# Optimization experiments

Hardware: AMD Instinct MI355X
Metric: run time of the kernel (lower is better)

Reference implementation:

```python
import jax, jax.numpy as jnp
import numpy as np

B, T, C = 4, 1024, 1024
H, LAT = 16, 512
E, K, F = 8, 2, 1024
N_SHARED = 2
EPS = 1e-6
HD = C // H


def setup_inputs() -> dict:
    key = jax.random.key(0)
    ks = jax.random.split(key, 20)
    s = 0.02
    inp = {
        'x': jax.random.normal(ks[0], (B, T, C), jnp.float32),
        'g_attn': jnp.ones((C,), jnp.float32),
        'wq': jax.random.normal(ks[1], (C, H * HD), jnp.float32) * s,
        'wkv_down': jax.random.normal(ks[2], (C, LAT), jnp.float32) * s,
        'wk_up': jax.random.normal(ks[3], (LAT, HD), jnp.float32) * s,
        'wv_up': jax.random.normal(ks[4], (LAT, HD), jnp.float32) * s,
        'wo': jax.random.normal(ks[5], (H * HD, C), jnp.float32) * s,
        'g_moe': jnp.ones((C,), jnp.float32),
        'wr': jax.random.normal(ks[6], (C, E), jnp.float32) * s,
        'rb': jnp.zeros((E,), jnp.float32),
        'e_w1': jax.random.normal(ks[7], (E, C, F), jnp.float32) * s,
        'e_w2': jax.random.normal(ks[8], (E, F, C), jnp.float32) * s,
        'e_w3': jax.random.normal(ks[9], (E, C, F), jnp.float32) * s,
        's_w1': jax.random.normal(ks[10], (C, F * N_SHARED), jnp.float32) * s,
        's_w2': jax.random.normal(ks[11], (F * N_SHARED, C), jnp.float32) * s,
        's_w3': jax.random.normal(ks[12], (C, F * N_SHARED), jnp.float32) * s,
    }
    return inp


def _rmsnorm(x, g):
    ms = jnp.mean(jnp.square(x), axis=-1, keepdims=True)
    return x * jax.lax.rsqrt(ms + EPS) * g


def reference(x, g_attn, wq, wkv_down, wk_up, wv_up, wo, g_moe, wr, rb,
              e_w1, e_w2, e_w3, s_w1, s_w2, s_w3):
    # ---- MLA attention (no rope / no kv-cache path: freqs_cis=None, start_pos=None) ----
    xn = _rmsnorm(x, g_attn)
    q = (xn @ wq).reshape(B, T, H, HD)          # [B,T,H,hd]
    kv = xn @ wkv_down                            # [B,T,LAT]
    k = kv @ wk_up                                # [B,T,hd] shared across heads
    v = kv @ wv_up                                # [B,T,hd]
    scores = jnp.einsum('bthd,bsd->bhts', q, k) / jnp.sqrt(jnp.float32(HD))
    causal = jnp.tril(jnp.ones((T, T), dtype=bool))
    scores = jnp.where(causal, scores, -jnp.inf)
    p = jax.nn.softmax(scores, axis=-1)
    y = jnp.einsum('bhts,bsd->bthd', p, v).reshape(B, T, C) @ wo
    h = x + y

    # ---- DeepSeekMoE: top-k routing + masked softmax + experts + shared experts ----
    hn = _rmsnorm(h, g_moe)
    N = B * T
    xf = hn.reshape(N, C)
    logits = (xf @ wr) * (1.0 / jnp.sqrt(jnp.float32(C)))   # original logits
    biased = logits + rb
    _, idx = jax.lax.top_k(biased, K)                        # [N,K]
    mask = jnp.zeros((N, E), dtype=bool).at[jnp.arange(N)[:, None], idx].set(True)
    # softmax over only the selected logits; unselected -> 0 weight
    wfull = jax.nn.softmax(jnp.where(mask, logits, -jnp.inf), axis=-1)  # [N,E]

    # experts: SwiGLU FFN per expert (original computes each expert on all tokens)
    hid = jnp.einsum('nd,edf->enf', xf, e_w1) * jax.nn.silu(jnp.einsum('nd,edf->enf', xf, e_w3))
    moe_out = jnp.einsum('enf,efd,ne->nd', hid, e_w2, wfull)  # weighted combine

    shared = ((xf @ s_w1) * jax.nn.silu(xf @ s_w3)) @ s_w2
    out = h + (moe_out + shared).reshape(B, T, C)
    return out
```

## Files before the change

kernel.cpp:

```cpp
#include <hip/hip_runtime.h>
#include <hip/hip_bf16.h>

using bf16 = __hip_bfloat16;
typedef __attribute__((ext_vector_type(8))) short short8;
typedef __attribute__((ext_vector_type(4))) float f32x4;

static __device__ __forceinline__ float bf2f(bf16 v) { return __bfloat162float(v); }
static __device__ __forceinline__ bf16 f2bf(float v) { return __float2bfloat16(v); }

constexpr int CB = 4, CT = 1024, CC = 1024, CH = 16, CHD = 64, CLAT = 512;
constexpr int CE = 8, CF = 1024, CNS = 2;
constexpr int NTOK = CB * CT;
constexpr int FUP = CE * CF + CNS * CF;

struct alignas(8) bf16x4 { bf16 a, b, c, d; };

__global__ void pack_t_kernel(const float* __restrict__ src, bf16* __restrict__ dst,
                              int K, int N, int lddst, long srcZ, long dstZ, long plane) {
  __shared__ float tile[32][33];
  src += (long)blockIdx.z * srcZ;
  dst += (long)blockIdx.z * dstZ;
  int k0 = blockIdx.y * 32, n0 = blockIdx.x * 32;
  int tx = threadIdx.x, ty = threadIdx.y;
#pragma unroll
  for (int i = 0; i < 32; i += 8) {
    int k = k0 + ty + i, n = n0 + tx;
    tile[ty + i][tx] = (k < K && n < N) ? src[(long)k * N + n] : 0.f;
  }
  __syncthreads();
#pragma unroll
  for (int i = 0; i < 32; i += 8) {
    int n = n0 + ty + i, k = k0 + tx;
    if (n < N && k < K) {
      float v = tile[tx][ty + i];
      bf16 hi = f2bf(v);
      long idx = (long)n * lddst + k;
      dst[idx] = hi;
      if (plane) dst[idx + plane] = f2bf(v - bf2f(hi));
    }
  }
}

template<bool SPLIT>
__global__ void rmsnorm_kernel(const float* __restrict__ x, const float* __restrict__ g,
                               bf16* __restrict__ ob, long plane) {
  int row = blockIdx.x;
  int t = threadIdx.x;
  const float4* xr = (const float4*)(x + (long)row * CC);
  float4 v = xr[t];
  float ss = v.x * v.x + v.y * v.y + v.z * v.z + v.w * v.w;
#pragma unroll
  for (int o = 32; o > 0; o >>= 1) ss += __shfl_down(ss, o);
  __shared__ float wsum[4];
  if ((t & 63) == 0) wsum[t >> 6] = ss;
  __syncthreads();
  float tot = wsum[0] + wsum[1] + wsum[2] + wsum[3];
  float r = rsqrtf(tot * (1.f / CC) + 1e-6f);
  const float4* gr = (const float4*)g;
  float4 gv = gr[t];
  float o0 = v.x * r * gv.x, o1 = v.y * r * gv.y, o2 = v.z * r * gv.z, o3 = v.w * r * gv.w;
  long base = (long)row * CC + t * 4;
  bf16x4 hv = {f2bf(o0), f2bf(o1), f2bf(o2), f2bf(o3)};
  *(bf16x4*)(ob + base) = hv;
  if (SPLIT) {
    bf16x4 lv = {f2bf(o0 - bf2f(hv.a)), f2bf(o1 - bf2f(hv.b)),
                 f2bf(o2 - bf2f(hv.c)), f2bf(o3 - bf2f(hv.d))};
    *(bf16x4*)(ob + plane + base) = lv;
  }
}

__global__ void router_kernel(const float* __restrict__ hb, const float* __restrict__ g,
                              const float* __restrict__ wr, const float* __restrict__ rb,
                              float* __restrict__ wf) {
  int n = blockIdx.x, l = threadIdx.x;
  const float* hrow = hb + (long)n * CC;
  float xs[16];
  float ss = 0.f;
#pragma unroll
  for (int i = 0; i < 16; i++) {
    float xv = hrow[i * 64 + l];
    xs[i] = xv;
    ss += xv * xv;
  }
#pragma unroll
  for (int o = 32; o > 0; o >>= 1) ss += __shfl_xor(ss, o);
  float r = rsqrtf(ss * (1.f / CC) + 1e-6f);
  float acc[CE];
#pragma unroll
  for (int e = 0; e < CE; e++) acc[e] = 0.f;
#pragma unroll
  for (int i = 0; i < 16; i++) {
    int c = i * 64 + l;
    float v = xs[i] * r * g[c];
    const float* w = wr + (long)c * CE;
#pragma unroll
    for (int e = 0; e < CE; e++) acc[e] += v * w[e];
  }
#pragma unroll
  for (int e = 0; e < CE; e++)
#pragma unroll
    for (int o = 32; o > 0; o >>= 1) acc[e] += __shfl_down(acc[e], o);
  if (l == 0) {
    float lg[CE], bi[CE];
#pragma unroll
    for (int e = 0; e < CE; e++) { lg[e] = acc[e] * (1.f / 32.f); bi[e] = lg[e] + rb[e]; }
    int i1 = 0;
#pragma unroll
    for (int e = 1; e < CE; e++) if (bi[e] > bi[i1]) i1 = e;
    int i2 = -1;
#pragma unroll
    for (int e = 0; e < CE; e++) if (e != i1 && (i2 < 0 || bi[e] > bi[i2])) i2 = e;
    float mx = fmaxf(lg[i1], lg[i2]);
    float e1 = expf(lg[i1] - mx), e2 = expf(lg[i2] - mx);
    float inv = 1.f / (e1 + e2);
#pragma unroll
    for (int e = 0; e < CE; e++) wf[(long)n * CE + e] = 0.f;
    wf[(long)n * CE + i1] = e1 * inv;
    wf[(long)n * CE + i2] = e2 * inv;
  }
}

__global__ void softmax_kernel(bf16* __restrict__ scp, long plane) {
  int wid = threadIdx.x >> 6, l = threadIdx.x & 63;
  long rowid = (long)blockIdx.x * 4 + wid;
  int t = (int)(rowid & (CT - 1));
  bf16* row = scp + rowid * CT;
  int len = t + 1;
  float v[16];
  float m = -1e30f;
#pragma unroll
  for (int ii = 0; ii < 16; ii++) {
    int i = ii * 64 + l;
    v[ii] = (i < len) ? (bf2f(row[i]) + bf2f(row[i + plane])) * 0.125f : -1e30f;
    m = fmaxf(m, v[ii]);
  }
#pragma unroll
  for (int o = 32; o > 0; o >>= 1) m = fmaxf(m, __shfl_xor(m, o));
  float s = 0.f;
#pragma unroll
  for (int ii = 0; ii < 16; ii++) { v[ii] = expf(v[ii] - m); s += v[ii]; }
#pragma unroll
  for (int o = 32; o > 0; o >>= 1) s += __shfl_xor(s, o);
  float inv = 1.f / s;
#pragma unroll
  for (int ii = 0; ii < 16; ii++) {
    int i = ii * 64 + l;
    float pv = v[ii] * inv;
    bf16 hi = f2bf(pv);
    row[i] = hi;
    row[i + plane] = f2bf(pv - bf2f(hi));
  }
}

constexpr int EPI_SPLIT = 1, EPI_ADD = 2, EPI_KV = 3, EPI_SWIGLU = 4;

template<int BN, int EPI, int MODE>
__global__ __launch_bounds__(256) void gemm_bt(
    const bf16* __restrict__ A, long lda, long planeA,
    const bf16* __restrict__ B1, const bf16* __restrict__ B3, long ldb,
    void* __restrict__ Cv, long ldc, long planeC,
    int M, int N, int K,
    int zdiv, long sAz1, long sAz2, long sBz1, long sBz2, long sCz1, long sCz2,
    const float* __restrict__ aux1, void* __restrict__ aux2, int causal) {
  constexpr int BM = 128, BK = 32;
  constexpr int PA = (MODE == 1) ? 2 : 1;
  constexpr int PB = (MODE == 0) ? 1 : 2;
  constexpr int WN = (BN == 128) ? 2 : 1;
  constexpr int WM = 4 / WN;
  constexpr int FM = BM / (16 * WM);
  constexpr int FN = BN / (16 * WN);
  constexpr int ITA = (BM * BK / 8) / 256;
  constexpr int ITB = (BN * BK / 8) / 256;
  constexpr int A3 = (MODE == 2) ? FM : 1;
  constexpr int B3N = (MODE == 2) ? FN : 1;

  __shared__ bf16 As[PA][BM][BK];
  __shared__ bf16 Bs[PB][BN][BK];

  int z = blockIdx.z;
  int z1 = z / zdiv, z2 = z % zdiv;
  long offA = (long)z1 * sAz1 + (long)z2 * sAz2;
  long offB = (long)z1 * sBz1 + (long)z2 * sBz2;
  long offC = (long)z1 * sCz1 + (long)z2 * sCz2;

  int m0 = blockIdx.y * BM;
  int n0 = blockIdx.x * BN;
  if (causal && n0 > m0 + (BM - 1)) return;

  int tid = threadIdx.x;
  int wid = tid >> 6, lane = tid & 63;
  int wrow = (wid / WN) * (BM / WM);
  int wcol = (wid % WN) * (BN / WN);
  int lr = lane & 15, lk8 = (lane >> 4) * 8;

  const bf16* Ap0 = A + offA;
  const bf16* Ap1 = Ap0 + planeA;
  const bf16* Bp0 = B1 + offB;
  const bf16* Bp1 = B3 + offB;

  f32x4 acc[FM][FN] = {};
  f32x4 acc3[A3][B3N] = {};

  for (int k0 = 0; k0 < K; k0 += BK) {
    __syncthreads();
#pragma unroll
    for (int p = 0; p < PA; p++) {
      const bf16* Ap = p ? Ap1 : Ap0;
#pragma unroll
      for (int i = 0; i < ITA; i++) {
        int c = i * 256 + wid * 64 + lane;
        int r = c >> 2;
        int kc = (c & 3) * 8;
        __builtin_amdgcn_global_load_lds(
            (const __attribute__((address_space(1))) void*)(const void*)(Ap + (long)(m0 + r) * lda + (k0 + kc)),
            (__attribute__((address_space(3))) void*)(void*)(&As[p][0][0] + (i * 256 + wid * 64) * 8),
            16, 0, 0);
      }
    }
#pragma unroll
    for (int p = 0; p < PB; p++) {
      const bf16* Bp = p ? Bp1 : Bp0;
#pragma unroll
      for (int i = 0; i < ITB; i++) {
        int c = i * 256 + wid * 64 + lane;
        int r = c >> 2;
        int kc = (c & 3) * 8;
        __builtin_amdgcn_global_load_lds(
            (const __attribute__((address_space(1))) void*)(const void*)(Bp + (long)(n0 + r) * ldb + (k0 + kc)),
            (__attribute__((address_space(3))) void*)(void*)(&Bs[p][0][0] + (i * 256 + wid * 64) * 8),
            16, 0, 0);
      }
    }
    __syncthreads();

    short8 av[PA][FM], bv[PB][FN];
#pragma unroll
    for (int p = 0; p < PA; p++)
#pragma unroll
      for (int m = 0; m < FM; m++)
        av[p][m] = *(const short8*)&As[p][wrow + m * 16 + lr][lk8];
#pragma unroll
    for (int p = 0; p < PB; p++)
#pragma unroll
      for (int n = 0; n < FN; n++)
        bv[p][n] = *(const short8*)&Bs[p][wcol + n * 16 + lr][lk8];

#pragma unroll
    for (int m = 0; m < FM; m++)
#pragma unroll
      for (int n = 0; n < FN; n++) {
        if constexpr (MODE == 0) {
          acc[m][n] = __builtin_amdgcn_mfma_f32_16x16x32_bf16(av[0][m], bv[0][n], acc[m][n], 0, 0, 0);
        } else if constexpr (MODE == 1) {
          acc[m][n] = __builtin_amdgcn_mfma_f32_16x16x32_bf16(av[0][m], bv[0][n], acc[m][n], 0, 0, 0);
          acc[m][n] = __builtin_amdgcn_mfma_f32_16x16x32_bf16(av[0][m], bv[1][n], acc[m][n], 0, 0, 0);
          acc[m][n] = __builtin_amdgcn_mfma_f32_16x16x32_bf16(av[1][m], bv[0][n], acc[m][n], 0, 0, 0);
        } else {
          acc[m][n]  = __builtin_amdgcn_mfma_f32_16x16x32_bf16(av[0][m], bv[0][n], acc[m][n], 0, 0, 0);
          acc3[m][n] = __builtin_amdgcn_mfma_f32_16x16x32_bf16(av[0][m], bv[1][n], acc3[m][n], 0, 0, 0);
        }
      }
  }

#pragma unroll
  for (int m = 0; m < FM; m++)
#pragma unroll
    for (int n = 0; n < FN; n++) {
      int col = n0 + wcol + n * 16 + lr;
      if (col < N) {
#pragma unroll
        for (int r = 0; r < 4; r++) {
          int row = m0 + wrow + m * 16 + (lane >> 4) * 4 + r;
          float val = acc[m][n][r];
          if constexpr (EPI == EPI_SPLIT) {
            bf16 hi = f2bf(val);
            long ci = offC + (long)row * ldc + col;
            ((bf16*)Cv)[ci] = hi;
            ((bf16*)Cv)[ci + planeC] = f2bf(val - bf2f(hi));
          } else if constexpr (EPI == EPI_ADD) {
            long ci = (long)row * ldc + col;
            ((float*)Cv)[ci] = aux1[ci] + val;
          } else if constexpr (EPI == EPI_KV) {
            bf16 hi = f2bf(val);
            bf16 lo = f2bf(val - bf2f(hi));
            if (col < CHD) {
              long ci = (long)row * CHD + col;
              ((bf16*)Cv)[ci] = hi;
              ((bf16*)Cv)[ci + 262144] = lo;
            } else {
              int d = col - CHD;
              long vi = ((long)(row >> 10) * CHD + d) * CT + (row & (CT - 1));
              ((bf16*)aux2)[vi] = hi;
              ((bf16*)aux2)[vi + 262144] = lo;
            }
          } else if constexpr (EPI == EPI_SWIGLU) {
            float g3 = (MODE == 2) ? acc3[m][n][r] : 0.f;
            float sl = g3 / (1.f + expf(-g3));
            float wt = (col < CE * CF) ? aux1[(long)row * CE + (col >> 10)] : 1.f;
            ((bf16*)Cv)[(long)row * ldc + col] = f2bf(val * sl * wt);
          }
        }
      }
    }
}

extern "C" void kernel_launch(void* const* d_in, const int* in_sizes, int n_in,
                              void* d_out, int out_size, void* d_ws, size_t ws_size,
                              hipStream_t stream) {
  (void)in_sizes; (void)n_in; (void)out_size; (void)ws_size;
  const float* x        = (const float*)d_in[0];
  const float* g_attn   = (const float*)d_in[1];
  const float* wq       = (const float*)d_in[2];
  const float* wkv_down = (const float*)d_in[3];
  const float* wk_up    = (const float*)d_in[4];
  const float* wv_up    = (const float*)d_in[5];
  const float* wo       = (const float*)d_in[6];
  const float* g_moe    = (const float*)d_in[7];
  const float* wr       = (const float*)d_in[8];
  const float* rb       = (const float*)d_in[9];
  const float* e_w1     = (const float*)d_in[10];
  const float* e_w2     = (const float*)d_in[11];
  const float* e_w3     = (const float*)d_in[12];
  const float* s_w1     = (const float*)d_in[13];
  const float* s_w2     = (const float*)d_in[14];
  const float* s_w3     = (const float*)d_in[15];
  float* out = (float*)d_out;

  char* base = (char*)d_ws;
  bf16*  WqT    = (bf16*)(base + 0);
  bf16*  WkvT   = (bf16*)(base + 4194304);
  bf16*  WkvupT = (bf16*)(base + 6291456);
  bf16*  WoT    = (bf16*)(base + 6553600);
  bf16*  W1T    = (bf16*)(base + 10747904);
  bf16*  W3T    = (bf16*)(base + 31719424);
  bf16*  W2T    = (bf16*)(base + 52690944);
  float* hb     = (float*)(base + 73662464);
  float* wful   = (float*)(base + 90439680);
  char*  AR     = base + 90570752;
  bf16* xn  = (bf16*)(AR + 0);
  bf16* qb  = (bf16*)(AR + 16777216);
  bf16* kb  = (bf16*)(AR + 33554432);
  bf16* vt  = (bf16*)(AR + 34603008);
  bf16* scp = (bf16*)(AR + 35651584);
  bf16* kvb = scp;
  bf16* yb  = xn;
  bf16* hnb = (bf16*)(AR + 0);
  bf16* hid = (bf16*)(AR + 8388608);

  dim3 pblk(32, 8);
  auto packl = [&](const float* src, bf16* dst, int K, int N, int ld, int Z,
                   long srcZ, long dstZ, long plane) {
    dim3 g((N + 31) / 32, (K + 31) / 32, Z);
    hipLaunchKernelGGL(pack_t_kernel, g, pblk, 0, stream, src, dst, K, N, ld, srcZ, dstZ, plane);
  };
  packl(wq, WqT, 1024, 1024, 1024, 1, 0, 0, 1048576);
  packl(wkv_down, WkvT, 1024, 512, 1024, 1, 0, 0, 524288);
  packl(wk_up, WkvupT, 512, 64, 512, 1, 0, 0, 65536);
  packl(wv_up, WkvupT + 64 * 512, 512, 64, 512, 1, 0, 0, 65536);
  packl(wo, WoT, 1024, 1024, 1024, 1, 0, 0, 1048576);
  packl(e_w1, W1T, 1024, 1024, 1024, 8, 1048576, 1048576, 0);
  packl(s_w1, W1T + 8192l * 1024, 1024, 2048, 1024, 1, 0, 0, 0);
  packl(e_w3, W3T, 1024, 1024, 1024, 8, 1048576, 1048576, 0);
  packl(s_w3, W3T + 8192l * 1024, 1024, 2048, 1024, 1, 0, 0, 0);
  packl(e_w2, W2T, 1024, 1024, FUP, 8, 1048576, 1024, 0);
  packl(s_w2, W2T + 8192, 2048, 1024, FUP, 1, 0, 0, 0);

  hipLaunchKernelGGL((rmsnorm_kernel<true>), dim3(NTOK), dim3(256), 0, stream,
                     x, g_attn, xn, 4194304l);

  hipLaunchKernelGGL((gemm_bt<128, EPI_SPLIT, 1>), dim3(8, 32, 1), dim3(256), 0, stream,
                     xn, 1024l, 4194304l, WqT, WqT + 1048576, 1024l,
                     (void*)qb, 1024l, 4194304l, 4096, 1024, 1024,
                     1, 0l, 0l, 0l, 0l, 0l, 0l, (const float*)nullptr, (void*)nullptr, 0);

  hipLaunchKernelGGL((gemm_bt<128, EPI_SPLIT, 1>), dim3(4, 32, 1), dim3(256), 0, stream,
                     xn, 1024l, 4194304l, WkvT, WkvT + 524288, 1024l,
                     (void*)kvb, 512l, 2097152l, 4096, 512, 1024,
                     1, 0l, 0l, 0l, 0l, 0l, 0l, (const float*)nullptr, (void*)nullptr, 0);

  hipLaunchKernelGGL((gemm_bt<128, EPI_KV, 1>), dim3(1, 32, 1), dim3(256), 0, stream,
                     kvb, 512l, 2097152l, WkvupT, WkvupT + 65536, 512l,
                     (void*)kb, 64l, 0l, 4096, 128, 512,
                     1, 0l, 0l, 0l, 0l, 0l, 0l, (const float*)nullptr, (void*)vt, 0);

  for (int b = 0; b < CB; b++) {
    hipLaunchKernelGGL((gemm_bt<128, EPI_SPLIT, 1>), dim3(8, 8, 16), dim3(256), 0, stream,
                       qb + (long)b * 1048576, 1024l, 4194304l,
                       kb + (long)b * 65536, kb + (long)b * 65536 + 262144, 64l,
                       (void*)scp, 1024l, 16777216l, 1024, 1024, 64,
                       16, 0l, 64l, 0l, 0l, 0l, 1048576l,
                       (const float*)nullptr, (void*)nullptr, 1);
    hipLaunchKernelGGL(softmax_kernel, dim3(4096), dim3(256), 0, stream, scp, 16777216l);
    hipLaunchKernelGGL((gemm_bt<64, EPI_SPLIT, 1>), dim3(1, 8, 16), dim3(256), 0, stream,
                       scp, 1024l, 16777216l,
                       vt + (long)b * 65536, vt + (long)b * 65536 + 262144, 1024l,
                       (void*)(yb + (long)b * 1048576), 1024l, 4194304l, 1024, 64, 1024,
                       16, 0l, 1048576l, 0l, 0l, 0l, 64l,
                       (const float*)nullptr, (void*)nullptr, 0);
  }

  hipLaunchKernelGGL((gemm_bt<128, EPI_ADD, 1>), dim3(8, 32, 1), dim3(256), 0, stream,
                     yb, 1024l, 4194304l, WoT, WoT + 1048576, 1024l,
                     (void*)hb, 1024l, 0l, 4096, 1024, 1024,
                     1, 0l, 0l, 0l, 0l, 0l, 0l, x, (void*)nullptr, 0);

  hipLaunchKernelGGL(router_kernel, dim3(NTOK), dim3(64), 0, stream, hb, g_moe, wr, rb, wful);
  hipLaunchKernelGGL((rmsnorm_kernel<false>), dim3(NTOK), dim3(256), 0, stream,
                     hb, g_moe, hnb, 0l);

  hipLaunchKernelGGL((gemm_bt<64, EPI_SWIGLU, 2>), dim3(FUP / 64, 32, 1), dim3(256), 0, stream,
                     hnb, 1024l, 0l, W1T, W3T, 1024l,
                     (void*)hid, (long)FUP, 0l, 4096, FUP, 1024,
                     1, 0l, 0l, 0l, 0l, 0l, 0l, wful, (void*)nullptr, 0);

  hipLaunchKernelGGL((gemm_bt<64, EPI_ADD, 0>), dim3(16, 32, 1), dim3(256), 0, stream,
                     hid, (long)FUP, 0l, W2T, W2T, (long)FUP,
                     (void*)out, 1024l, 0l, 4096, 1024, FUP,
                     1, 0l, 0l, 0l, 0l, 0l, 0l, hb, (void*)nullptr, 0);
}
```

Baseline: 1.172 ms.

## Switch split-precision planes from bf16 to scaled fp16 and skip causal PV tiles

Replaces the bf16 hi/lo split representation with fp16 hi plus a low plane scaled by 2048, so the residual keeps more precision in fp16 MFMAs. The split-mode GEMM now accumulates the cross terms in a separate accumulator and rescales them in the epilogue. Softmax only writes probabilities up to the next 128-column boundary, and the P·V GEMM stops its K loop at the causal diagonal, skipping masked work. This risks fp16 overflow or range issues on unnormalized activations and relies on stale-but-unused scores beyond the written region being skipped.

```diff
diff --git a/kernel.cpp b/kernel.cpp
--- a/kernel.cpp
+++ b/kernel.cpp
@@ -1,21 +1,26 @@
 #include <hip/hip_runtime.h>
-#include <hip/hip_bf16.h>
-
-using bf16 = __hip_bfloat16;
-typedef __attribute__((ext_vector_type(8))) short short8;
+#include <hip/hip_fp16.h>
+
+using f16 = __half;
+typedef _Float16 half8 __attribute__((ext_vector_type(8)));
 typedef __attribute__((ext_vector_type(4))) float f32x4;
 
-static __device__ __forceinline__ float bf2f(bf16 v) { return __bfloat162float(v); }
-static __device__ __forceinline__ bf16 f2bf(float v) { return __float2bfloat16(v); }
+static __device__ __forceinline__ float h2f(f16 v) { return __half2float(v); }
+static __device__ __forceinline__ f16 f2h(float v) { return __float2half(v); }
+
+static __device__ __forceinline__ f16 loss(float v, f16 hi) {
+  return f2h((v - h2f(hi)) * 2048.f);
+}
 
 constexpr int CB = 4, CT = 1024, CC = 1024, CH = 16, CHD = 64, CLAT = 512;
 constexpr int CE = 8, CF = 1024, CNS = 2;
 constexpr int NTOK = CB * CT;
 constexpr int FUP = CE * CF + CNS * CF;
-
-struct alignas(8) bf16x4 { bf16 a, b, c, d; };
-
-__global__ void pack_t_kernel(const float* __restrict__ src, bf16* __restrict__ dst,
+constexpr float INV2K = 1.f / 2048.f;
+
+struct alignas(8) f16x4s { f16 a, b, c, d; };
+
+__global__ void pack_t_kernel(const float* __restrict__ src, f16* __restrict__ dst,
                               int K, int N, int lddst, long srcZ, long dstZ, long plane) {
   __shared__ float tile[32][33];
   src += (long)blockIdx.z * srcZ;
@@ -33,17 +38,17 @@
     int n = n0 + ty + i, k = k0 + tx;
     if (n < N && k < K) {
       float v = tile[tx][ty + i];
-      bf16 hi = f2bf(v);
+      f16 hi = f2h(v);
       long idx = (long)n * lddst + k;
       dst[idx] = hi;
-      if (plane) dst[idx + plane] = f2bf(v - bf2f(hi));
+      if (plane) dst[idx + plane] = loss(v, hi);
     }
   }
 }
 
 template<bool SPLIT>
 __global__ void rmsnorm_kernel(const float* __restrict__ x, const float* __restrict__ g,
-                               bf16* __restrict__ ob, long plane) {
+                               f16* __restrict__ ob, long plane) {
   int row = blockIdx.x;
   int t = threadIdx.x;
   const float4* xr = (const float4*)(x + (long)row * CC);
@@ -60,12 +65,11 @@
   float4 gv = gr[t];
   float o0 = v.x * r * gv.x, o1 = v.y * r * gv.y, o2 = v.z * r * gv.z, o3 = v.w * r * gv.w;
   long base = (long)row * CC + t * 4;
-  bf16x4 hv = {f2bf(o0), f2bf(o1), f2bf(o2), f2bf(o3)};
-  *(bf16x4*)(ob + base) = hv;
+  f16x4s hv = {f2h(o0), f2h(o1), f2h(o2), f2h(o3)};
+  *(f16x4s*)(ob + base) = hv;
   if (SPLIT) {
-    bf16x4 lv = {f2bf(o0 - bf2f(hv.a)), f2bf(o1 - bf2f(hv.b)),
-                 f2bf(o2 - bf2f(hv.c)), f2bf(o3 - bf2f(hv.d))};
-    *(bf16x4*)(ob + plane + base) = lv;
+    f16x4s lv = {loss(o0, hv.a), loss(o1, hv.b), loss(o2, hv.c), loss(o3, hv.d)};
+    *(f16x4s*)(ob + plane + base) = lv;
   }
 }
 
@@ -120,18 +124,19 @@
   }
 }
 
-__global__ void softmax_kernel(bf16* __restrict__ scp, long plane) {
+__global__ void softmax_kernel(f16* __restrict__ scp, long plane) {
   int wid = threadIdx.x >> 6, l = threadIdx.x & 63;
   long rowid = (long)blockIdx.x * 4 + wid;
   int t = (int)(rowid & (CT - 1));
-  bf16* row = scp + rowid * CT;
+  f16* row = scp + rowid * CT;
   int len = t + 1;
+  int wlen = ((t >> 7) + 1) << 7;
   float v[16];
   float m = -1e30f;
 #pragma unroll
   for (int ii = 0; ii < 16; ii++) {
     int i = ii * 64 + l;
-    v[ii] = (i < len) ? (bf2f(row[i]) + bf2f(row[i + plane])) * 0.125f : -1e30f;
+    v[ii] = (i < len) ? (h2f(row[i]) + h2f(row[i + plane]) * INV2K) * 0.125f : -1e30f;
     m = fmaxf(m, v[ii]);
   }
 #pragma unroll
@@ -145,10 +150,12 @@
 #pragma unroll
   for (int ii = 0; ii < 16; ii++) {
     int i = ii * 64 + l;
-    float pv = v[ii] * inv;
-    bf16 hi = f2bf(pv);
-    row[i] = hi;
-    row[i + plane] = f2bf(pv - bf2f(hi));
+    if (i < wlen) {
+      float pv = v[ii] * inv;
+      f16 hi = f2h(pv);
+      row[i] = hi;
+      row[i + plane] = loss(pv, hi);
+    }
   }
 }
 
@@ -156,8 +163,8 @@
 
 template<int BN, int EPI, int MODE>
 __global__ __launch_bounds__(256) void gemm_bt(
-    const bf16* __restrict__ A, long lda, long planeA,
-    const bf16* __restrict__ B1, const bf16* __restrict__ B3, long ldb,
+    const f16* __restrict__ A, long lda, long planeA,
+    const f16* __restrict__ B1, const f16* __restrict__ B3, long ldb,
     void* __restrict__ Cv, long ldc, long planeC,
     int M, int N, int K,
     int zdiv, long sAz1, long sAz2, long sBz1, long sBz2, long sCz1, long sCz2,
@@ -171,11 +178,11 @@
   constexpr int FN = BN / (16 * WN);
   constexpr int ITA = (BM * BK / 8) / 256;
   constexpr int ITB = (BN * BK / 8) / 256;
-  constexpr int A3 = (MODE == 2) ? FM : 1;
-  constexpr int B3N = (MODE == 2) ? FN : 1;
-
-  __shared__ bf16 As[PA][BM][BK];
-  __shared__ bf16 Bs[PB][BN][BK];
+  constexpr int X2 = (MODE != 0) ? FM : 1;
+  constexpr int X2N = (MODE != 0) ? FN : 1;
+
+  __shared__ f16 As[PA][BM][BK];
+  __shared__ f16 Bs[PB][BN][BK];
 
   int z = blockIdx.z;
   int z1 = z / zdiv, z2 = z % zdiv;
@@ -185,7 +192,7 @@
 
   int m0 = blockIdx.y * BM;
   int n0 = blockIdx.x * BN;
-  if (causal && n0 > m0 + (BM - 1)) return;
+  if (causal == 1 && n0 > m0 + (BM - 1)) return;
 
   int tid = threadIdx.x;
   int wid = tid >> 6, lane = tid & 63;
@@ -193,19 +200,21 @@
   int wcol = (wid % WN) * (BN / WN);
   int lr = lane & 15, lk8 = (lane >> 4) * 8;
 
-  const bf16* Ap0 = A + offA;
-  const bf16* Ap1 = Ap0 + planeA;
-  const bf16* Bp0 = B1 + offB;
-  const bf16* Bp1 = B3 + offB;
+  const f16* Ap0 = A + offA;
+  const f16* Ap1 = Ap0 + planeA;
+  const f16* Bp0 = B1 + offB;
+  const f16* Bp1 = B3 + offB;
 
   f32x4 acc[FM][FN] = {};
-  f32x4 acc3[A3][B3N] = {};
-
-  for (int k0 = 0; k0 < K; k0 += BK) {
+  f32x4 acc2[X2][X2N] = {};
+
+  int Kend = (causal == 2) ? ((m0 + BM < K) ? (m0 + BM) : K) : K;
+
+  for (int k0 = 0; k0 < Kend; k0 += BK) {
     __syncthreads();
 #pragma unroll
     for (int p = 0; p < PA; p++) {
-      const bf16* Ap = p ? Ap1 : Ap0;
+      const f16* Ap = p ? Ap1 : Ap0;
 #pragma unroll
       for (int i = 0; i < ITA; i++) {
         int c = i * 256 + wid * 64 + lane;
@@ -219,7 +228,7 @@
     }
 #pragma unroll
     for (int p = 0; p < PB; p++) {
-      const bf16* Bp = p ? Bp1 : Bp0;
+      const f16* Bp = p ? Bp1 : Bp0;
 #pragma unroll
       for (int i = 0; i < ITB; i++) {
         int c = i * 256 + wid * 64 + lane;
@@ -233,31 +242,31 @@
     }
     __syncthreads();
 
-    short8 av[PA][FM], bv[PB][FN];
+    half8 av[PA][FM], bv[PB][FN];
 #pragma unroll
     for (int p = 0; p < PA; p++)
 #pragma unroll
       for (int m = 0; m < FM; m++)
-        av[p][m] = *(const short8*)&As[p][wrow + m * 16 + lr][lk8];
+        av[p][m] = *(const half8*)&As[p][wrow + m * 16 + lr][lk8];
 #pragma unroll
     for (int p = 0; p < PB; p++)
 #pragma unroll
       for (int n = 0; n < FN; n++)
-        bv[p][n] = *(const short8*)&Bs[p][wcol + n * 16 + lr][lk8];
+        bv[p][n] = *(const half8*)&Bs[p][wcol + n * 16 + lr][lk8];
 
 #pragma unroll
     for (int m = 0; m < FM; m++)
 #pragma unroll
       for (int n = 0; n < FN; n++) {
         if constexpr (MODE == 0) {
-          acc[m][n] = __builtin_amdgcn_mfma_f32_16x16x32_bf16(av[0][m], bv[0][n], acc[m][n], 0, 0, 0);
+          acc[m][n] = __builtin_amdgcn_mfma_f32_16x16x32_f16(av[0][m], bv[0][n], acc[m][n], 0, 0, 0);
         } else if constexpr (MODE == 1) {
-          acc[m][n] = __builtin_amdgcn_mfma_f32_16x16x32_bf16(av[0][m], bv[0][n], acc[m][n], 0, 0, 0);
-          acc[m][n] = __builtin_amdgcn_mfma_f32_16x16x32_bf16(av[0][m], bv[1][n], acc[m][n], 0, 0, 0);
-          acc[m][n] = __builtin_amdgcn_mfma_f32_16x16x32_bf16(av[1][m], bv[0][n], acc[m][n], 0, 0, 0);
+          acc[m][n]  = __builtin_amdgcn_mfma_f32_16x16x32_f16(av[0][m], bv[0][n], acc[m][n], 0, 0, 0);
+          acc2[m][n] = __builtin_amdgcn_mfma_f32_16x16x32_f16(av[0][m], bv[1][n], acc2[m][n], 0, 0, 0);
+          acc2[m][n] = __builtin_amdgcn_mfma_f32_16x16x32_f16(av[1][m], bv[0][n], acc2[m][n], 0, 0, 0);
         } else {
-          acc[m][n]  = __builtin_amdgcn_mfma_f32_16x16x32_bf16(av[0][m], bv[0][n], acc[m][n], 0, 0, 0);
-          acc3[m][n] = __builtin_amdgcn_mfma_f32_16x16x32_bf16(av[0][m], bv[1][n], acc3[m][n], 0, 0, 0);
+          acc[m][n]  = __builtin_amdgcn_mfma_f32_16x16x32_f16(av[0][m], bv[0][n], acc[m][n], 0, 0, 0);
+          acc2[m][n] = __builtin_amdgcn_mfma_f32_16x16x32_f16(av[0][m], bv[1][n], acc2[m][n], 0, 0, 0);
         }
       }
   }
@@ -272,32 +281,33 @@
         for (int r = 0; r < 4; r++) {
           int row = m0 + wrow + m * 16 + (lane >> 4) * 4 + r;
           float val = acc[m][n][r];
+          if constexpr (MODE == 1) val += acc2[m][n][r] * INV2K;
           if constexpr (EPI == EPI_SPLIT) {
-            bf16 hi = f2bf(val);
+            f16 hi = f2h(val);
             long ci = offC + (long)row * ldc + col;
-            ((bf16*)Cv)[ci] = hi;
-            ((bf16*)Cv)[ci + planeC] = f2bf(val - bf2f(hi));
+            ((f16*)Cv)[ci] = hi;
+            ((f16*)Cv)[ci + planeC] = loss(val, hi);
           } else if constexpr (EPI == EPI_ADD) {
             long ci = (long)row * ldc + col;
             ((float*)Cv)[ci] = aux1[ci] + val;
           } else if constexpr (EPI == EPI_KV) {
-            bf16 hi = f2bf(val);
-            bf16 lo = f2bf(val - bf2f(hi));
+            f16 hi = f2h(val);
+            f16 lo = loss(val, hi);
             if (col < CHD) {
               long ci = (long)row * CHD + col;
-              ((bf16*)Cv)[ci] = hi;
-              ((bf16*)Cv)[ci + 262144] = lo;
+              ((f16*)Cv)[ci] = hi;
+              ((f16*)Cv)[ci + 262144] = lo;
             } else {
               int d = col - CHD;
               long vi = ((long)(row >> 10) * CHD + d) * CT + (row & (CT - 1));
-              ((bf16*)aux2)[vi] = hi;
-              ((bf16*)aux2)[vi + 262144] = lo;
+              ((f16*)aux2)[vi] = hi;
+              ((f16*)aux2)[vi + 262144] = lo;
             }
           } else if constexpr (EPI == EPI_SWIGLU) {
-            float g3 = (MODE == 2) ? acc3[m][n][r] : 0.f;
+            float g3 = (MODE == 2) ? acc2[m][n][r] : 0.f;
             float sl = g3 / (1.f + expf(-g3));
             float wt = (col < CE * CF) ? aux1[(long)row * CE + (col >> 10)] : 1.f;
-            ((bf16*)Cv)[(long)row * ldc + col] = f2bf(val * sl * wt);
+            ((f16*)Cv)[(long)row * ldc + col] = f2h(val * sl * wt);
           }
         }
       }
@@ -327,28 +337,28 @@
   float* out = (float*)d_out;
 
   char* base = (char*)d_ws;
-  bf16*  WqT    = (bf16*)(base + 0);
-  bf16*  WkvT   = (bf16*)(base + 4194304);
-  bf16*  WkvupT = (bf16*)(base + 6291456);
-  bf16*  WoT    = (bf16*)(base + 6553600);
-  bf16*  W1T    = (bf16*)(base + 10747904);
-  bf16*  W3T    = (bf16*)(base + 31719424);
-  bf16*  W2T    = (bf16*)(base + 52690944);
+  f16*   WqT    = (f16*)(base + 0);
+  f16*   WkvT   = (f16*)(base + 4194304);
+  f16*   WkvupT = (f16*)(base + 6291456);
+  f16*   WoT    = (f16*)(base + 6553600);
+  f16*   W1T    = (f16*)(base + 10747904);
+  f16*   W3T    = (f16*)(base + 31719424);
+  f16*   W2T    = (f16*)(base + 52690944);
   float* hb     = (float*)(base + 73662464);
   float* wful   = (float*)(base + 90439680);
   char*  AR     = base + 90570752;
-  bf16* xn  = (bf16*)(AR + 0);
-  bf16* qb  = (bf16*)(AR + 16777216);
-  bf16* kb  = (bf16*)(AR + 33554432);
-  bf16* vt  = (bf16*)(AR + 34603008);
-  bf16* scp = (bf16*)(AR + 35651584);
-  bf16* kvb = scp;
-  bf16* yb  = xn;
-  bf16* hnb = (bf16*)(AR + 0);
-  bf16* hid = (bf16*)(AR + 8388608);
+  f16* xn  = (f16*)(AR + 0);
+  f16* qb  = (f16*)(AR + 16777216);
+  f16* kb  = (f16*)(AR + 33554432);
+  f16* vt  = (f16*)(AR + 34603008);
+  f16* scp = (f16*)(AR + 35651584);
+  f16* kvb = scp;
+  f16* yb  = xn;
+  f16* hnb = (f16*)(AR + 0);
+  f16* hid = (f16*)(AR + 8388608);
 
   dim3 pblk(32, 8);
-  auto packl = [&](const float* src, bf16* dst, int K, int N, int ld, int Z,
+  auto packl = [&](const float* src, f16* dst, int K, int N, int ld, int Z,
                    long srcZ, long dstZ, long plane) {
     dim3 g((N + 31) / 32, (K + 31) / 32, Z);
     hipLaunchKernelGGL(pack_t_kernel, g, pblk, 0, stream, src, dst, K, N, ld, srcZ, dstZ, plane);
@@ -396,7 +406,7 @@
                        vt + (long)b * 65536, vt + (long)b * 65536 + 262144, 1024l,
                        (void*)(yb + (long)b * 1048576), 1024l, 4194304l, 1024, 64, 1024,
                        16, 0l, 1048576l, 0l, 0l, 0l, 64l,
-                       (const float*)nullptr, (void*)nullptr, 0);
+                       (const float*)nullptr, (void*)nullptr, 2);
   }
 
   hipLaunchKernelGGL((gemm_bt<128, EPI_ADD, 1>), dim3(8, 32, 1), dim3(256), 0, stream,
```

Result: slower. 1.223 ms (+4.4%).
